# Optimization experiments

Measured on AMD Instinct MI355X. Metric: run time of the kernel, lower is better.

The kernel has to match this reference:

```python
import jax, jax.numpy as jnp
import numpy as np

T, D, H, E = 8192, 1024, 512, 8
BLK = 32  # MXFP8 scaling block size along the contraction dim


def setup_inputs() -> dict:
    key = jax.random.key(0)
    k1, k2, k3, k4 = jax.random.split(key, 4)
    # qdata: values representable-ish in e4m3 (we use small normal floats)
    output_e4m3 = jax.random.normal(k1, (T, D), dtype=jnp.float32)
    # e8m0 scales are powers of two, one per 32-element block along dim
    output_scales_e8m0 = jnp.exp2(
        jax.random.randint(k2, (T, D // BLK), -2, 3).astype(jnp.float32)
    )
    # uniform token distribution across experts (tokens are expert-contiguous)
    num_tokens_per_expert = jnp.full((E,), T // E, dtype=jnp.int32)
    expert_padded_offsets = jnp.zeros((E,), dtype=jnp.int32)  # unused by forward body
    w13 = jax.random.normal(k3, (E, 2 * H, D), dtype=jnp.float32) * 0.02
    w2 = jax.random.normal(k4, (E, D, H), dtype=jnp.float32) * 0.02
    return {
        "output_e4m3": output_e4m3,
        "output_scales_e8m0": output_scales_e8m0,
        "num_tokens_per_expert": num_tokens_per_expert,
        "expert_padded_offsets": expert_padded_offsets,
        "w13": w13,
        "w2": w2,
    }


def reference(output_e4m3, output_scales_e8m0, num_tokens_per_expert,
              expert_padded_offsets, w13, w2):
    # Dequantize MXFP8: qdata * per-block e8m0 scale, blocks of 32 along dim.
    scales = jnp.repeat(output_scales_e8m0, BLK, axis=-1)  # [T, D]
    x = output_e4m3 * scales  # [T, D] high-precision reference activations
    # Grouped GEMM 1: tokens are expert-contiguous with uniform group sizes,
    # so the ragged grouped matmul reduces to a batched einsum per expert.
    tpe = T // E
    xg = x.reshape(E, tpe, D)                       # [E, tpe, D]
    h13 = jnp.einsum("etd,ehd->eth", xg, w13)       # [E, tpe, 2H]
    h1, h3 = h13[..., :H], h13[..., H:]
    h = jax.nn.silu(h1) * h3                        # fused SiLU-gate
    # Grouped GEMM 2
    out = jnp.einsum("eth,edh->etd", h, w2)         # [E, tpe, D]
    return out.reshape(T, D)
```

## Files before the change

### kernel.cpp

```cpp
#include <hip/hip_runtime.h>
#include <hip/hip_bf16.h>

#define T_TOK 8192
#define DDIM  1024
#define HDIM  512
#define NE    8
#define TPE   (T_TOK / NE)

typedef __attribute__((ext_vector_type(4))) float floatx4;
typedef __attribute__((ext_vector_type(8))) short bf16x8;

__device__ __forceinline__ unsigned short f2bf(float f) {
    union { float f; unsigned int u; } v;
    v.f = f;
    unsigned int u = v.u;
    unsigned int r = u + 0x7FFFu + ((u >> 16) & 1u);
    return (unsigned short)(r >> 16);
}

__device__ __forceinline__ unsigned int cvt_pk_bf16(float lo, float hi) {
    unsigned int r;
    asm("v_cvt_pk_bf16_f32 %0, %1, %2" : "=v"(r) : "v"(lo), "v"(hi));
    return r;
}

__device__ __forceinline__ void gld_lds16(const void* g, void* l) {
    __builtin_amdgcn_global_load_lds(
        (const __attribute__((address_space(1))) unsigned int*)g,
        (__attribute__((address_space(3))) unsigned int*)l, 16, 0, 0);
}

__global__ __launch_bounds__(256)
void convert_w13_kernel(const float* __restrict__ W13,
                        unsigned short* __restrict__ W13b)
{
    const int NT13 = (NE * 2 * HDIM * DDIM) / 4;
    const int stride = gridDim.x * blockDim.x;
    for (int i = blockIdx.x * blockDim.x + threadIdx.x; i < NT13; i += stride) {
        float4 v = reinterpret_cast<const float4*>(W13)[i];
        ushort4 b;
        b.x = f2bf(v.x); b.y = f2bf(v.y); b.z = f2bf(v.z); b.w = f2bf(v.w);
        reinterpret_cast<ushort4*>(W13b)[i] = b;
    }
}

__device__ __forceinline__ int xcd_swizzle_512(int raw) {
    return (raw & 7) * 64 + (raw >> 3);
}


__global__ __launch_bounds__(256, 2)
void gemm1_silu_kernel(const float* __restrict__ X,
                       const float* __restrict__ S,
                       const unsigned short* __restrict__ W13b,
                       __hip_bfloat16* __restrict__ Hout)
{
    const int bid = xcd_swizzle_512(blockIdx.x);
    const int e  = bid >> 6;
    const int mt = (bid >> 3) & 7;
    const int nt = bid & 7;
    const int tok0 = e * TPE + mt * 128;
    const unsigned short* __restrict__ We = W13b + (size_t)e * (2 * HDIM) * DDIM;

    __shared__ __hip_bfloat16 sA[2][128][64];
    __shared__ __hip_bfloat16 sB[2][128][64];

    const int tid  = threadIdx.x;
    const int lane = tid & 63;
    const int wave = tid >> 6;
    const int wr = wave >> 1;
    const int wc = wave & 1;
    const int lr = lane & 15;
    const int sw0 = ((lane >> 4) ^ (lane & 7));

    floatx4 acc1[4][2] = {};
    floatx4 acc3[4][2] = {};

    const int srow0 = (tid >> 3);
    const int c8    = (tid & 7) * 8;
    const int dcol  = (tid & 7) * 8;
    const int swcol = ((tid & 7) ^ (srow0 & 7)) * 8;

    float4 rA[8]; float rs[4];

    auto LOADA = [&](int kk) {
        const int k0 = kk * 64;
        #pragma unroll
        for (int j = 0; j < 4; ++j) {
            int row = srow0 + j * 32;
            const float* p = &X[(size_t)(tok0 + row) * DDIM + k0 + c8];
            rA[2*j]   = *reinterpret_cast<const float4*>(p);
            rA[2*j+1] = *reinterpret_cast<const float4*>(p + 4);
            rs[j] = S[(size_t)(tok0 + row) * (DDIM / 32) + ((k0 + c8) >> 5)];
        }
    };
    auto STAGEB = [&](int kk, int buf) {
        const int k0 = kk * 64;
        #pragma unroll
        for (int j = 0; j < 4; ++j) {
            int row = srow0 + j * 32;
            int wrow = (j < 2) ? (nt * 64 + row)
                               : (HDIM + nt * 64 + (row - 64));
            gld_lds16(&We[(size_t)wrow * DDIM + k0 + swcol],
                      &sB[buf][row][dcol]);
        }
    };
    auto WRITEA = [&](int buf) {
        #pragma unroll
        for (int j = 0; j < 4; ++j) {
            int row = srow0 + j * 32;
            float sc = rs[j];
            uint4 w;
            w.x = cvt_pk_bf16(rA[2*j].x * sc,   rA[2*j].y * sc);
            w.y = cvt_pk_bf16(rA[2*j].z * sc,   rA[2*j].w * sc);
            w.z = cvt_pk_bf16(rA[2*j+1].x * sc, rA[2*j+1].y * sc);
            w.w = cvt_pk_bf16(rA[2*j+1].z * sc, rA[2*j+1].w * sc);
            *reinterpret_cast<uint4*>(&sA[buf][row][swcol]) = w;
        }
    };
    auto COMPUTE = [&](int buf) {
        #pragma unroll
        for (int ks = 0; ks < 2; ++ks) {
            const int rc = (sw0 ^ (ks << 2)) << 3;
            bf16x8 a[4], b1[2], b3[2];
            #pragma unroll
            for (int m = 0; m < 4; ++m)
                a[m] = *reinterpret_cast<const bf16x8*>(&sA[buf][wr * 64 + m * 16 + lr][rc]);
            #pragma unroll
            for (int n = 0; n < 2; ++n) {
                b1[n] = *reinterpret_cast<const bf16x8*>(&sB[buf][wc * 32 + n * 16 + lr][rc]);
                b3[n] = *reinterpret_cast<const bf16x8*>(&sB[buf][64 + wc * 32 + n * 16 + lr][rc]);
            }
            #pragma unroll
            for (int m = 0; m < 4; ++m)
                #pragma unroll
                for (int n = 0; n < 2; ++n) {
                    acc1[m][n] = __builtin_amdgcn_mfma_f32_16x16x32_bf16(a[m], b1[n], acc1[m][n], 0, 0, 0);
                    acc3[m][n] = __builtin_amdgcn_mfma_f32_16x16x32_bf16(a[m], b3[n], acc3[m][n], 0, 0, 0);
                }
        }
    };

    LOADA(0);
    __builtin_amdgcn_sched_barrier(0);
    STAGEB(0, 0);
    __builtin_amdgcn_sched_barrier(0);
    for (int kk = 0; kk < DDIM / 64 - 1; ++kk) {
        const int buf = kk & 1;
        asm volatile("s_waitcnt vmcnt(4)" ::: "memory");
        __builtin_amdgcn_sched_barrier(0);
        WRITEA(buf);
        __builtin_amdgcn_sched_barrier(0);
        LOADA(kk + 1);
        __builtin_amdgcn_sched_barrier(0);
        STAGEB(kk + 1, buf ^ 1);
        __builtin_amdgcn_sched_barrier(0);
        asm volatile("s_waitcnt vmcnt(16) lgkmcnt(0)" ::: "memory");
        __builtin_amdgcn_sched_barrier(0);
        __builtin_amdgcn_s_barrier();
        COMPUTE(buf);
        __builtin_amdgcn_s_barrier();
    }
    asm volatile("s_waitcnt vmcnt(4)" ::: "memory");
    __builtin_amdgcn_sched_barrier(0);
    WRITEA(1);
    asm volatile("s_waitcnt vmcnt(0) lgkmcnt(0)" ::: "memory");
    __builtin_amdgcn_sched_barrier(0);
    __builtin_amdgcn_s_barrier();
    COMPUTE(1);

    const int hcol0 = nt * 64 + wc * 32;
    #pragma unroll
    for (int m = 0; m < 4; ++m) {
        #pragma unroll
        for (int n = 0; n < 2; ++n) {
            #pragma unroll
            for (int i = 0; i < 4; ++i) {
                int row = tok0 + wr * 64 + m * 16 + (lane >> 4) * 4 + i;
                int col = hcol0 + n * 16 + (lane & 15);
                float h1 = acc1[m][n][i];
                float h3 = acc3[m][n][i];
                float sig = 1.0f / (1.0f + __expf(-h1));
                Hout[(size_t)row * HDIM + col] = __float2bfloat16(h1 * sig * h3);
            }
        }
    }
}

__global__ __launch_bounds__(256, 2)
void gemm2_kernel(const __hip_bfloat16* __restrict__ Hin,
                  const float* __restrict__ W2,
                  float* __restrict__ Out)
{
    const int bid = xcd_swizzle_512(blockIdx.x);
    const int e  = bid >> 6;
    const int nt = (bid >> 3) & 7;
    const int mt = bid & 7;
    const int tok0 = e * TPE + mt * 128;
    const float* __restrict__ We = W2 + (size_t)e * DDIM * HDIM;

    __shared__ __hip_bfloat16 sA[2][128][64];
    __shared__ __hip_bfloat16 sB[2][128][64];

    const int tid  = threadIdx.x;
    const int lane = tid & 63;
    const int wave = tid >> 6;
    const int wr = wave >> 1;
    const int wc = wave & 1;
    const int lr = lane & 15;
    const int sw0 = ((lane >> 4) ^ (lane & 7));

    floatx4 acc[4][4] = {};

    const int srow0 = (tid >> 3);
    const int c8    = (tid & 7) * 8;
    const int dcol  = (tid & 7) * 8;
    const int swcol = ((tid & 7) ^ (srow0 & 7)) * 8;

    float4 rB[8];

    auto LOADB = [&](int kk) {
        const int k0 = kk * 64;
        #pragma unroll
        for (int j = 0; j < 4; ++j) {
            int row = srow0 + j * 32;
            const float* p = &We[(size_t)(nt * 128 + row) * HDIM + k0 + c8];
            rB[2*j]   = *reinterpret_cast<const float4*>(p);
            rB[2*j+1] = *reinterpret_cast<const float4*>(p + 4);
        }
    };
    auto STAGEA = [&](int kk, int buf) {
        const int k0 = kk * 64;
        #pragma unroll
        for (int j = 0; j < 4; ++j) {
            int row = srow0 + j * 32;
            gld_lds16(&Hin[(size_t)(tok0 + row) * HDIM + k0 + swcol],
                      &sA[buf][row][dcol]);
        }
    };
    auto WRITEB = [&](int buf) {
        #pragma unroll
        for (int j = 0; j < 4; ++j) {
            int row = srow0 + j * 32;
            uint4 w;
            w.x = cvt_pk_bf16(rB[2*j].x,   rB[2*j].y);
            w.y = cvt_pk_bf16(rB[2*j].z,   rB[2*j].w);
            w.z = cvt_pk_bf16(rB[2*j+1].x, rB[2*j+1].y);
            w.w = cvt_pk_bf16(rB[2*j+1].z, rB[2*j+1].w);
            *reinterpret_cast<uint4*>(&sB[buf][row][swcol]) = w;
        }
    };
    auto COMPUTE = [&](int buf) {
        #pragma unroll
        for (int ks = 0; ks < 2; ++ks) {
            const int rc = (sw0 ^ (ks << 2)) << 3;
            bf16x8 a[4], b[4];
            #pragma unroll
            for (int m = 0; m < 4; ++m)
                a[m] = *reinterpret_cast<const bf16x8*>(&sA[buf][wr * 64 + m * 16 + lr][rc]);
            #pragma unroll
            for (int n = 0; n < 4; ++n)
                b[n] = *reinterpret_cast<const bf16x8*>(&sB[buf][wc * 64 + n * 16 + lr][rc]);
            #pragma unroll
            for (int m = 0; m < 4; ++m)
                #pragma unroll
                for (int n = 0; n < 4; ++n)
                    acc[m][n] = __builtin_amdgcn_mfma_f32_16x16x32_bf16(a[m], b[n], acc[m][n], 0, 0, 0);
        }
    };

    LOADB(0);
    __builtin_amdgcn_sched_barrier(0);
    STAGEA(0, 0);
    __builtin_amdgcn_sched_barrier(0);
    for (int kk = 0; kk < HDIM / 64 - 1; ++kk) {
        const int buf = kk & 1;
        asm volatile("s_waitcnt vmcnt(4)" ::: "memory");
        __builtin_amdgcn_sched_barrier(0);
        WRITEB(buf);
        __builtin_amdgcn_sched_barrier(0);
        LOADB(kk + 1);
        __builtin_amdgcn_sched_barrier(0);
        STAGEA(kk + 1, buf ^ 1);
        __builtin_amdgcn_sched_barrier(0);
        asm volatile("s_waitcnt vmcnt(12) lgkmcnt(0)" ::: "memory");
        __builtin_amdgcn_sched_barrier(0);
        __builtin_amdgcn_s_barrier();
        COMPUTE(buf);
        __builtin_amdgcn_s_barrier();
    }
    asm volatile("s_waitcnt vmcnt(4)" ::: "memory");
    __builtin_amdgcn_sched_barrier(0);
    WRITEB(1);
    asm volatile("s_waitcnt vmcnt(0) lgkmcnt(0)" ::: "memory");
    __builtin_amdgcn_sched_barrier(0);
    __builtin_amdgcn_s_barrier();
    COMPUTE(1);

    const int dcol0 = nt * 128 + wc * 64;
    #pragma unroll
    for (int m = 0; m < 4; ++m) {
        #pragma unroll
        for (int n = 0; n < 4; ++n) {
            #pragma unroll
            for (int i = 0; i < 4; ++i) {
                int row = tok0 + wr * 64 + m * 16 + (lane >> 4) * 4 + i;
                int col = dcol0 + n * 16 + (lane & 15);
                Out[(size_t)row * DDIM + col] = acc[m][n][i];
            }
        }
    }
}

extern "C" void kernel_launch(void* const* d_in, const int* in_sizes, int n_in,
                              void* d_out, int out_size, void* d_ws, size_t ws_size,
                              hipStream_t stream) {
    const float* X   = (const float*)d_in[0];
    const float* S   = (const float*)d_in[1];
    const float* W13 = (const float*)d_in[4];
    const float* W2  = (const float*)d_in[5];
    float* Out = (float*)d_out;

    unsigned short* W13b = (unsigned short*)d_ws;
    __hip_bfloat16* Hb   = (__hip_bfloat16*)(W13b + (size_t)NE * 2 * HDIM * DDIM);

    convert_w13_kernel<<<2048, 256, 0, stream>>>(W13, W13b);
    gemm1_silu_kernel<<<NE * 8 * 8, 256, 0, stream>>>(X, S, W13b, Hb);
    gemm2_kernel<<<NE * 8 * 8, 256, 0, stream>>>(Hb, W2, Out);
}
```

Measured before the change: 58.05 us.

## Pre-convert activations to bf16 instead of weights; stage fp32 W13 via registers

Swaps which operand is pre-converted. A separate kernel now dequantizes X with its scales to bf16, writing into the output buffer as scratch, and GEMM1 loads it with direct global-to-LDS copies. The fp32 W13 is loaded into registers, converted in-kernel, and double-buffered two tiles ahead. Each weight tile is still read by the 8 M-tiles of its expert, so fp32 weight traffic grows relative to bf16, while the pre-pass shrinks from 16M to 8M elements. It also reuses d_out as temporary storage, which depends on GEMM2 overwriting it later.

```diff
diff --git a/kernel.cpp b/kernel.cpp
--- a/kernel.cpp
+++ b/kernel.cpp
@@ -31,16 +31,20 @@
 }
 
 __global__ __launch_bounds__(256)
-void convert_w13_kernel(const float* __restrict__ W13,
-                        unsigned short* __restrict__ W13b)
+void convert_x_kernel(const float* __restrict__ X, const float* __restrict__ S,
+                      unsigned short* __restrict__ Xb)
 {
-    const int NT13 = (NE * 2 * HDIM * DDIM) / 4;
+    const int NTX = (T_TOK * DDIM) / 4;
     const int stride = gridDim.x * blockDim.x;
-    for (int i = blockIdx.x * blockDim.x + threadIdx.x; i < NT13; i += stride) {
-        float4 v = reinterpret_cast<const float4*>(W13)[i];
+    for (int i = blockIdx.x * blockDim.x + threadIdx.x; i < NTX; i += stride) {
+        int row = i >> 8;
+        int c4  = i & 255;
+        float4 v = reinterpret_cast<const float4*>(X)[i];
+        float sc = S[row * (DDIM / 32) + (c4 >> 3)];
         ushort4 b;
-        b.x = f2bf(v.x); b.y = f2bf(v.y); b.z = f2bf(v.z); b.w = f2bf(v.w);
-        reinterpret_cast<ushort4*>(W13b)[i] = b;
+        b.x = f2bf(v.x * sc); b.y = f2bf(v.y * sc);
+        b.z = f2bf(v.z * sc); b.w = f2bf(v.w * sc);
+        reinterpret_cast<ushort4*>(Xb)[i] = b;
     }
 }
 
@@ -50,9 +54,8 @@
 
 
 __global__ __launch_bounds__(256, 2)
-void gemm1_silu_kernel(const float* __restrict__ X,
-                       const float* __restrict__ S,
-                       const unsigned short* __restrict__ W13b,
+void gemm1_silu_kernel(const unsigned short* __restrict__ Xb,
+                       const float* __restrict__ W13,
                        __hip_bfloat16* __restrict__ Hout)
 {
     const int bid = xcd_swizzle_512(blockIdx.x);
@@ -60,7 +63,7 @@
     const int mt = (bid >> 3) & 7;
     const int nt = bid & 7;
     const int tok0 = e * TPE + mt * 128;
-    const unsigned short* __restrict__ We = W13b + (size_t)e * (2 * HDIM) * DDIM;
+    const float* __restrict__ We = W13 + (size_t)e * (2 * HDIM) * DDIM;
 
     __shared__ __hip_bfloat16 sA[2][128][64];
     __shared__ __hip_bfloat16 sB[2][128][64];
@@ -79,43 +82,42 @@
     const int srow0 = (tid >> 3);
     const int c8    = (tid & 7) * 8;
     const int dcol  = (tid & 7) * 8;
-    const int swcol = ((tid & 7) ^ (srow0 & 7)) * 8;
-
-    float4 rA[8]; float rs[4];
-
-    auto LOADA = [&](int kk) {
-        const int k0 = kk * 64;
-        #pragma unroll
-        for (int j = 0; j < 4; ++j) {
-            int row = srow0 + j * 32;
-            const float* p = &X[(size_t)(tok0 + row) * DDIM + k0 + c8];
-            rA[2*j]   = *reinterpret_cast<const float4*>(p);
-            rA[2*j+1] = *reinterpret_cast<const float4*>(p + 4);
-            rs[j] = S[(size_t)(tok0 + row) * (DDIM / 32) + ((k0 + c8) >> 5)];
-        }
-    };
-    auto STAGEB = [&](int kk, int buf) {
+    const int gcol  = ((tid & 7) ^ (srow0 & 7)) * 8;
+    const int swcol = gcol;
+
+    float4 rB0[8], rB1[8];
+
+    auto LOADB = [&](int kk, float4* rB) {
         const int k0 = kk * 64;
         #pragma unroll
         for (int j = 0; j < 4; ++j) {
             int row = srow0 + j * 32;
             int wrow = (j < 2) ? (nt * 64 + row)
                                : (HDIM + nt * 64 + (row - 64));
-            gld_lds16(&We[(size_t)wrow * DDIM + k0 + swcol],
-                      &sB[buf][row][dcol]);
-        }
-    };
-    auto WRITEA = [&](int buf) {
-        #pragma unroll
-        for (int j = 0; j < 4; ++j) {
-            int row = srow0 + j * 32;
-            float sc = rs[j];
+            const float* p = &We[(size_t)wrow * DDIM + k0 + c8];
+            rB[2*j]   = *reinterpret_cast<const float4*>(p);
+            rB[2*j+1] = *reinterpret_cast<const float4*>(p + 4);
+        }
+    };
+    auto STAGEA = [&](int kk, int buf) {
+        const int k0 = kk * 64;
+        #pragma unroll
+        for (int j = 0; j < 4; ++j) {
+            int row = srow0 + j * 32;
+            gld_lds16(&Xb[(size_t)(tok0 + row) * DDIM + k0 + gcol],
+                      &sA[buf][row][dcol]);
+        }
+    };
+    auto WRITEB = [&](int buf, const float4* rB) {
+        #pragma unroll
+        for (int j = 0; j < 4; ++j) {
+            int row = srow0 + j * 32;
             uint4 w;
-            w.x = cvt_pk_bf16(rA[2*j].x * sc,   rA[2*j].y * sc);
-            w.y = cvt_pk_bf16(rA[2*j].z * sc,   rA[2*j].w * sc);
-            w.z = cvt_pk_bf16(rA[2*j+1].x * sc, rA[2*j+1].y * sc);
-            w.w = cvt_pk_bf16(rA[2*j+1].z * sc, rA[2*j+1].w * sc);
-            *reinterpret_cast<uint4*>(&sA[buf][row][swcol]) = w;
+            w.x = cvt_pk_bf16(rB[2*j].x,   rB[2*j].y);
+            w.y = cvt_pk_bf16(rB[2*j].z,   rB[2*j].w);
+            w.z = cvt_pk_bf16(rB[2*j+1].x, rB[2*j+1].y);
+            w.w = cvt_pk_bf16(rB[2*j+1].z, rB[2*j+1].w);
+            *reinterpret_cast<uint4*>(&sB[buf][row][swcol]) = w;
         }
     };
     auto COMPUTE = [&](int buf) {
@@ -141,29 +143,51 @@
         }
     };
 
-    LOADA(0);
-    __builtin_amdgcn_sched_barrier(0);
-    STAGEB(0, 0);
-    __builtin_amdgcn_sched_barrier(0);
-    for (int kk = 0; kk < DDIM / 64 - 1; ++kk) {
-        const int buf = kk & 1;
-        asm volatile("s_waitcnt vmcnt(4)" ::: "memory");
-        __builtin_amdgcn_sched_barrier(0);
-        WRITEA(buf);
-        __builtin_amdgcn_sched_barrier(0);
-        LOADA(kk + 1);
-        __builtin_amdgcn_sched_barrier(0);
-        STAGEB(kk + 1, buf ^ 1);
-        __builtin_amdgcn_sched_barrier(0);
-        asm volatile("s_waitcnt vmcnt(16) lgkmcnt(0)" ::: "memory");
-        __builtin_amdgcn_sched_barrier(0);
-        __builtin_amdgcn_s_barrier();
-        COMPUTE(buf);
-        __builtin_amdgcn_s_barrier();
-    }
-    asm volatile("s_waitcnt vmcnt(4)" ::: "memory");
-    __builtin_amdgcn_sched_barrier(0);
-    WRITEA(1);
+    LOADB(0, rB0);
+    __builtin_amdgcn_sched_barrier(0);
+    LOADB(1, rB1);
+    __builtin_amdgcn_sched_barrier(0);
+    STAGEA(0, 0);
+    __builtin_amdgcn_sched_barrier(0);
+    asm volatile("s_waitcnt vmcnt(12)" ::: "memory");
+    __builtin_amdgcn_sched_barrier(0);
+
+    for (int t = 0; t < DDIM / 64 - 2; t += 2) {
+        WRITEB(0, rB0);
+        __builtin_amdgcn_sched_barrier(0);
+        LOADB(t + 2, rB0);
+        __builtin_amdgcn_sched_barrier(0);
+        STAGEA(t + 1, 1);
+        __builtin_amdgcn_sched_barrier(0);
+        asm volatile("s_waitcnt vmcnt(12) lgkmcnt(0)" ::: "memory");
+        __builtin_amdgcn_sched_barrier(0);
+        __builtin_amdgcn_s_barrier();
+        COMPUTE(0);
+        __builtin_amdgcn_s_barrier();
+        WRITEB(1, rB1);
+        __builtin_amdgcn_sched_barrier(0);
+        LOADB(t + 3, rB1);
+        __builtin_amdgcn_sched_barrier(0);
+        STAGEA(t + 2, 0);
+        __builtin_amdgcn_sched_barrier(0);
+        asm volatile("s_waitcnt vmcnt(12) lgkmcnt(0)" ::: "memory");
+        __builtin_amdgcn_sched_barrier(0);
+        __builtin_amdgcn_s_barrier();
+        COMPUTE(1);
+        __builtin_amdgcn_s_barrier();
+    }
+
+    WRITEB(0, rB0);
+    __builtin_amdgcn_sched_barrier(0);
+    STAGEA(15, 1);
+    __builtin_amdgcn_sched_barrier(0);
+    asm volatile("s_waitcnt vmcnt(4) lgkmcnt(0)" ::: "memory");
+    __builtin_amdgcn_sched_barrier(0);
+    __builtin_amdgcn_s_barrier();
+    COMPUTE(0);
+    __builtin_amdgcn_s_barrier();
+    WRITEB(1, rB1);
+    __builtin_amdgcn_sched_barrier(0);
     asm volatile("s_waitcnt vmcnt(0) lgkmcnt(0)" ::: "memory");
     __builtin_amdgcn_sched_barrier(0);
     __builtin_amdgcn_s_barrier();
@@ -321,10 +345,10 @@
     const float* W2  = (const float*)d_in[5];
     float* Out = (float*)d_out;
 
-    unsigned short* W13b = (unsigned short*)d_ws;
-    __hip_bfloat16* Hb   = (__hip_bfloat16*)(W13b + (size_t)NE * 2 * HDIM * DDIM);
-
-    convert_w13_kernel<<<2048, 256, 0, stream>>>(W13, W13b);
-    gemm1_silu_kernel<<<NE * 8 * 8, 256, 0, stream>>>(X, S, W13b, Hb);
+    __hip_bfloat16* Hb = (__hip_bfloat16*)d_ws;
+    unsigned short* Xb = (unsigned short*)d_out;
+
+    convert_x_kernel<<<2048, 256, 0, stream>>>(X, S, Xb);
+    gemm1_silu_kernel<<<NE * 8 * 8, 256, 0, stream>>>(Xb, W13, Hb);
     gemm2_kernel<<<NE * 8 * 8, 256, 0, stream>>>(Hb, W2, Out);
 }
```

After: 56.11 us. 3.3% less time.
